# Kernel tuning notes

Hardware: AMD Instinct MI355X
Metric: run time of the kernel (lower is better)

The kernel has to match this reference:

```python
import jax, jax.numpy as jnp
import numpy as np

B, N, D, K = 32, 196, 1024, 512  # batch, tokens (14x14), feature dim, prototypes
EPS = 1e-8  # torch F.cosine_similarity default eps


def setup_inputs() -> dict:
    key = jax.random.key(0)
    ks = jax.random.split(key, 8)
    z = jax.random.normal(ks[0], (B, N, D), jnp.float32)
    prototypes = jax.random.normal(ks[1], (K, D), jnp.float32)  # nn.Parameter(randn)
    gate_w = jax.random.normal(ks[2], (2 * D, D), jnp.float32) * 0.02  # Linear(2D->D), stored [in,out]
    gate_b = jnp.zeros((D,), jnp.float32)
    dec_w = jax.random.normal(ks[3], (D, 7 * 7 * 512), jnp.float32) * 0.02
    dec_b = jnp.zeros((7 * 7 * 512,), jnp.float32)
    ct1_w = jax.random.normal(ks[4], (512, 256, 4, 4), jnp.float32) * 0.02  # torch [in,out,kh,kw]
    ct1_b = jnp.zeros((256,), jnp.float32)
    ct2_w = jax.random.normal(ks[5], (256, 3, 4, 4), jnp.float32) * 0.02
    ct2_b = jnp.zeros((3,), jnp.float32)
    return dict(z=z, prototypes=prototypes, gate_w=gate_w, gate_b=gate_b,
                dec_w=dec_w, dec_b=dec_b, ct1_w=ct1_w, ct1_b=ct1_b,
                ct2_w=ct2_w, ct2_b=ct2_b)


def _conv_transpose(x, w, b):
    # ConvTranspose2d(k=4, stride=2, pad=1) == conv with lhs_dilation=2,
    # padding k-1-pad=2, spatially-flipped kernel, torch weight layout [in,out,kh,kw] -> IOHW.
    wf = jnp.flip(w, (2, 3))
    y = jax.lax.conv_general_dilated(
        x, wf, window_strides=(1, 1), padding=((2, 2), (2, 2)),
        lhs_dilation=(2, 2), dimension_numbers=("NCHW", "IOHW", "NCHW"))
    return y + b[None, :, None, None]


def reference(z, prototypes, gate_w, gate_b, dec_w, dec_b, ct1_w, ct1_b, ct2_w, ct2_b):
    # MemoryBank: cosine similarity of every token against every prototype
    zn = jnp.linalg.norm(z, axis=-1, keepdims=True)            # [B,N,1]
    pn = jnp.linalg.norm(prototypes, axis=-1)                  # [K]
    dots = jnp.einsum('bnd,kd->bnk', z, prototypes)            # [B,N,K]
    sim = dots / jnp.maximum(zn * pn[None, None, :], EPS)
    attn = jax.nn.softmax(sim, axis=-1)                        # [B,N,K]
    z_hat = jnp.einsum('bnk,kd->bnd', attn, prototypes)        # [B,N,D]
    # GatedFusion: sigmoid gate over concat(z, z_hat)
    gate = jax.nn.sigmoid(jnp.concatenate([z, z_hat], axis=-1) @ gate_w + gate_b)
    z_fused = gate * z + (1.0 - gate) * z_hat                  # [B,N,D]
    # Decoder (original reshape is shape-inconsistent; pool tokens -> [B,D])
    pooled = z_fused.mean(axis=1)                              # [B,D]
    h = (pooled @ dec_w + dec_b).reshape(-1, 512, 7, 7)
    h = jax.nn.relu(_conv_transpose(h, ct1_w, ct1_b))          # [B,256,14,14]
    x_recon = _conv_transpose(h, ct2_w, ct2_b)                 # [B,3,28,28]
    return x_recon, attn
```

## Files before the change

kernel.cpp:

```cpp
#include <hip/hip_runtime.h>
#include <cstdint>
#include <cstddef>
#include <cmath>

#define EPS_COS 1e-8f

typedef unsigned short u16;
typedef __attribute__((ext_vector_type(8))) short short8v;
typedef __attribute__((ext_vector_type(4))) short short4v;
typedef __attribute__((ext_vector_type(4))) float f32x4;

__device__ __forceinline__ u16 f2bf(float x) {
    unsigned int u = __float_as_uint(x);
    return (u16)((u + 0x7FFFu + ((u >> 16) & 1u)) >> 16);
}
__device__ __forceinline__ float bf2f(u16 h) {
    return __uint_as_float(((unsigned int)h) << 16);
}

__global__ __launch_bounds__(256) void norm_cvt_kernel(const float* __restrict__ src,
                                                       u16* __restrict__ dst, int dstStride,
                                                       float* __restrict__ norms) {
    int r = blockIdx.x;
    int t = threadIdx.x;
    const float4 v = *reinterpret_cast<const float4*>(&src[(size_t)r * 1024 + t * 4]);
    short4v o;
    o[0] = f2bf(v.x); o[1] = f2bf(v.y); o[2] = f2bf(v.z); o[3] = f2bf(v.w);
    *reinterpret_cast<short4v*>(&dst[(size_t)r * dstStride + t * 4]) = o;
    float ss = v.x * v.x + v.y * v.y + v.z * v.z + v.w * v.w;
#pragma unroll
    for (int off = 32; off > 0; off >>= 1) ss += __shfl_down(ss, off);
    __shared__ float red[4];
    int wave = t >> 6, lane = t & 63;
    if (lane == 0) red[wave] = ss;
    __syncthreads();
    if (t == 0) norms[r] = sqrtf(red[0] + red[1] + red[2] + red[3]);
}

__global__ __launch_bounds__(256) void transpose_cvt_kernel(const float* __restrict__ src,
                                                            u16* __restrict__ dst,
                                                            int R, int C) {
    __shared__ float tile[64][65];
    int c0 = blockIdx.x * 64, r0 = blockIdx.y * 64;
    int t = threadIdx.x;
#pragma unroll
    for (int j = 0; j < 16; ++j) {
        int idx = j * 256 + t;
        int r = idx >> 6, c = idx & 63;
        tile[r][c] = src[(size_t)(r0 + r) * C + c0 + c];
    }
    __syncthreads();
#pragma unroll
    for (int j = 0; j < 16; ++j) {
        int idx = j * 256 + t;
        int c = idx >> 6, r = idx & 63;
        dst[(size_t)(c0 + c) * R + r0 + r] = f2bf(tile[r][c]);
    }
}

__global__ __launch_bounds__(256) void prep_kernel(u16* __restrict__ hp,
                                                   const float* __restrict__ ct1w,
                                                   u16* __restrict__ wt,
                                                   const float* __restrict__ ct2w,
                                                   u16* __restrict__ wpad,
                                                   float* __restrict__ pooled) {
    int idx = blockIdx.x * 256 + threadIdx.x;
    if (idx < 165888) {
        short8v zv = {0, 0, 0, 0, 0, 0, 0, 0};
        *reinterpret_cast<short8v*>(hp + (size_t)idx * 8) = zv;
    } else if (idx < 165888 + 131072) {
        int i = idx - 165888;
        int oc = i & 255, ic = i >> 8;
        float v[16];
#pragma unroll
        for (int j = 0; j < 16; ++j) v[j] = ct1w[(size_t)i * 16 + j];
#pragma unroll
        for (int pp = 0; pp < 4; ++pp) {
            int py = pp >> 1, px = pp & 1;
#pragma unroll
            for (int tap = 0; tap < 4; ++tap) {
                int ty = tap >> 1, tx = tap & 1;
                int ky = (1 - py) + 2 * ty;
                int kx = (1 - px) + 2 * tx;
                wt[((size_t)(pp * 256 + oc)) * 2048 + ic * 4 + tap] = f2bf(v[ky * 4 + kx]);
            }
        }
    } else if (idx < 165888 + 131072 + 16384) {
        int i = idx - 165888 - 131072;
        int ic = i & 255;
        int col = i >> 8;
        float v = 0.0f;
        if (col < 48) {
            int kx = col & 3, ky = (col >> 2) & 3, oc = col >> 4;
            v = ct2w[((size_t)ic * 3 + oc) * 16 + ky * 4 + kx];
        }
        wpad[i] = f2bf(v);
    } else {
        int i = idx - 165888 - 131072 - 16384;
        *reinterpret_cast<f32x4*>(pooled + (size_t)i * 4) = (f32x4){0.f, 0.f, 0.f, 0.f};
    }
}

template <int FM, int FN, int EPI, bool SWZ>
__global__ __launch_bounds__(256) void mfma_gemm_kernel(
    const u16* __restrict__ A, int sA, size_t zsA,
    const u16* __restrict__ B, int sB, size_t zsB,
    int M, int N, int K,
    float* __restrict__ Cf,
    u16* __restrict__ Cb, int sCb,
    const float* __restrict__ bias,
    const u16* __restrict__ zbf,
    const u16* __restrict__ zhbf, int szh,
    float* __restrict__ outf) {
    constexpr int BM = FM * 32, BN = FN * 32;
    constexpr int NA = BM / 32;
    constexpr int NB = BN / 32;
    __shared__ __align__(16) u16 As[BM * 64];
    __shared__ __align__(16) u16 Bs[BN * 64];
    int bx = blockIdx.x, by = blockIdx.y;
    if (SWZ) {
        int gx = gridDim.x;
        int nwg = gx * gridDim.y;
        int lb = by * gx + bx;
        int flat = (lb & 7) * (nwg >> 3) + (lb >> 3);
        bx = flat % gx;
        by = flat / gx;
    }
    A += (size_t)blockIdx.z * zsA;
    B += (size_t)blockIdx.z * zsB;
    const int t = threadIdx.x;
    const int lane = t & 63;
    const int wid = t >> 6;
    const int wm = wid >> 1, wn = wid & 1;
    const int m0 = bx * BM, n0 = by * BN;
    const int g = lane >> 4, lr = lane & 15;

    f32x4 acc[FM][FN];
#pragma unroll
    for (int i = 0; i < FM; ++i)
#pragma unroll
        for (int j = 0; j < FN; ++j) acc[i][j] = (f32x4){0.f, 0.f, 0.f, 0.f};

    short8v ra[NA], rb[NB];
#pragma unroll
    for (int j = 0; j < NA; ++j) {
        int c = j * 256 + t, row = c >> 3, ck = c & 7;
        ra[j] = *reinterpret_cast<const short8v*>(A + (size_t)(m0 + row) * sA + ck * 8);
    }
#pragma unroll
    for (int j = 0; j < NB; ++j) {
        int c = j * 256 + t, row = c >> 3, ck = c & 7;
        rb[j] = *reinterpret_cast<const short8v*>(B + (size_t)(n0 + row) * sB + ck * 8);
    }

    for (int k0 = 0; k0 < K; k0 += 64) {
        __syncthreads();
#pragma unroll
        for (int j = 0; j < NA; ++j) {
            int c = j * 256 + t, row = c >> 3, ck = c & 7;
            *reinterpret_cast<short8v*>(As + row * 64 + ((ck ^ (row & 7)) << 3)) = ra[j];
        }
#pragma unroll
        for (int j = 0; j < NB; ++j) {
            int c = j * 256 + t, row = c >> 3, ck = c & 7;
            *reinterpret_cast<short8v*>(Bs + row * 64 + ((ck ^ (row & 7)) << 3)) = rb[j];
        }
        __syncthreads();
        if (k0 + 64 < K) {
#pragma unroll
            for (int j = 0; j < NA; ++j) {
                int c = j * 256 + t, row = c >> 3, ck = c & 7;
                ra[j] = *reinterpret_cast<const short8v*>(A + (size_t)(m0 + row) * sA + k0 + 64 + ck * 8);
            }
#pragma unroll
            for (int j = 0; j < NB; ++j) {
                int c = j * 256 + t, row = c >> 3, ck = c & 7;
                rb[j] = *reinterpret_cast<const short8v*>(B + (size_t)(n0 + row) * sB + k0 + 64 + ck * 8);
            }
        }
#pragma unroll
        for (int kk = 0; kk < 2; ++kk) {
            short8v af[FM], bfr[FN];
#pragma unroll
            for (int fm = 0; fm < FM; ++fm) {
                int row = wm * (FM * 16) + fm * 16 + lr;
                int rc = (kk * 4 + g) ^ (row & 7);
                af[fm] = *reinterpret_cast<const short8v*>(As + row * 64 + rc * 8);
            }
#pragma unroll
            for (int fn = 0; fn < FN; ++fn) {
                int col = wn * (FN * 16) + fn * 16 + lr;
                int rc = (kk * 4 + g) ^ (col & 7);
                bfr[fn] = *reinterpret_cast<const short8v*>(Bs + col * 64 + rc * 8);
            }
#pragma unroll
            for (int fm = 0; fm < FM; ++fm)
#pragma unroll
                for (int fn = 0; fn < FN; ++fn)
                    acc[fm][fn] = __builtin_amdgcn_mfma_f32_16x16x32_bf16(
                        af[fm], bfr[fn], acc[fm][fn], 0, 0, 0);
        }
    }

    if (EPI == 2) {
#pragma unroll
        for (int fn = 0; fn < FN; ++fn) {
            int col = n0 + wn * (FN * 16) + fn * 16 + lr;
            int base = m0 + wm * (FM * 16) + g * 4;
            int b0 = base / 196;
            float p0 = 0.f, p1 = 0.f;
#pragma unroll
            for (int fm = 0; fm < FM; ++fm) {
#pragma unroll
                for (int r = 0; r < 4; ++r) {
                    int row = base + fm * 16 + r;
                    float v = acc[fm][fn][r];
                    float gs = 1.0f / (1.0f + __expf(-(v + bias[col])));
                    float zv = bf2f(zbf[(size_t)row * szh + col]);
                    float zh = bf2f(zhbf[(size_t)row * szh + col]);
                    float fused = gs * zv + (1.0f - gs) * zh;
                    bool same = (row / 196) == b0;
                    p0 += same ? fused : 0.f;
                    p1 += same ? 0.f : fused;
                }
            }
            atomicAdd(&outf[(size_t)b0 * 1024 + col], p0);
            if (p1 != 0.f) atomicAdd(&outf[(size_t)(b0 + 1) * 1024 + col], p1);
        }
    } else {
#pragma unroll
        for (int fm = 0; fm < FM; ++fm) {
#pragma unroll
            for (int fn = 0; fn < FN; ++fn) {
#pragma unroll
                for (int r = 0; r < 4; ++r) {
                    int row = m0 + wm * (FM * 16) + fm * 16 + g * 4 + r;
                    int col = n0 + wn * (FN * 16) + fn * 16 + lr;
                    float v = acc[fm][fn][r];
                    if (EPI == 0) {
                        Cf[(size_t)row * N + col] = v;
                    } else if (EPI == 1) {
                        Cb[(size_t)row * sCb + col] = f2bf(v);
                    } else {
                        if (row < 1568) {
                            float vv = fmaxf(v + bias[col], 0.0f);
                            int bb = row / 49, ss = row - bb * 49;
                            Cb[(((size_t)bb * 4 + blockIdx.z) * 49 + ss) * 256 + col] = f2bf(vv);
                        }
                    }
                }
            }
        }
    }
}

__global__ __launch_bounds__(256) void softmax_kernel(const float* __restrict__ dots,
                                                      const float* __restrict__ zn,
                                                      const float* __restrict__ pn,
                                                      float* __restrict__ attn,
                                                      u16* __restrict__ attn_bf) {
    int m = blockIdx.x;
    int t = threadIdx.x;
    float zm = zn[m];
    float d0 = dots[(size_t)m * 512 + t];
    float d1 = dots[(size_t)m * 512 + t + 256];
    float v0 = d0 / fmaxf(zm * pn[t], EPS_COS);
    float v1 = d1 / fmaxf(zm * pn[t + 256], EPS_COS);
    float mx = fmaxf(v0, v1);
#pragma unroll
    for (int off = 32; off > 0; off >>= 1) mx = fmaxf(mx, __shfl_down(mx, off));
    __shared__ float red[8];
    int wave = t >> 6, lane = t & 63;
    if (lane == 0) red[wave] = mx;
    __syncthreads();
    if (t == 0) red[4] = fmaxf(fmaxf(red[0], red[1]), fmaxf(red[2], red[3]));
    __syncthreads();
    mx = red[4];
    float e0 = expf(v0 - mx), e1 = expf(v1 - mx);
    float s = e0 + e1;
#pragma unroll
    for (int off = 32; off > 0; off >>= 1) s += __shfl_down(s, off);
    if (lane == 0) red[wave] = s;
    __syncthreads();
    if (t == 0) red[5] = 1.0f / (red[0] + red[1] + red[2] + red[3]);
    __syncthreads();
    float r = red[5];
    float a0 = e0 * r, a1 = e1 * r;
    attn[(size_t)m * 512 + t] = a0;
    attn[(size_t)m * 512 + t + 256] = a1;
    attn_bf[(size_t)m * 512 + t] = f2bf(a0);
    attn_bf[(size_t)m * 512 + t + 256] = f2bf(a1);
}

#define DEC_KC 64
__global__ __launch_bounds__(256) void dec_split_kernel(const float* __restrict__ pooled,
                                                        const float* __restrict__ dec_w,
                                                        float* __restrict__ partial) {
    const int t = threadIdx.x;
    const int lane = t & 63;
    const int wv = t >> 6;
    const int c = blockIdx.x * 256 + lane * 4;
    const int kc = blockIdx.y;
    __shared__ float pl[32][DEC_KC];
    for (int i = t; i < 32 * DEC_KC; i += 256) {
        int b = i >> 6, kk = i & (DEC_KC - 1);
        pl[b][kk] = pooled[(size_t)b * 1024 + kc * DEC_KC + kk] * (1.0f / 196.0f);
    }
    __syncthreads();
    f32x4 acc[8];
#pragma unroll
    for (int j = 0; j < 8; ++j) acc[j] = (f32x4){0.f, 0.f, 0.f, 0.f};
    const float* wp = dec_w + (size_t)(kc * DEC_KC) * 25088 + c;
#pragma unroll 8
    for (int k = 0; k < DEC_KC; ++k) {
        f32x4 w4 = *reinterpret_cast<const f32x4*>(wp + (size_t)k * 25088);
#pragma unroll
        for (int j = 0; j < 8; ++j) {
            float pv = pl[wv * 8 + j][k];
            acc[j].x = fmaf(pv, w4.x, acc[j].x);
            acc[j].y = fmaf(pv, w4.y, acc[j].y);
            acc[j].z = fmaf(pv, w4.z, acc[j].z);
            acc[j].w = fmaf(pv, w4.w, acc[j].w);
        }
    }
#pragma unroll
    for (int j = 0; j < 8; ++j) {
        int b = wv * 8 + j;
        *reinterpret_cast<f32x4*>(partial + ((size_t)kc * 32 + b) * 25088 + c) = acc[j];
    }
}

__global__ __launch_bounds__(256) void dec_reduce_kernel(const float* __restrict__ partial,
                                                         const float* __restrict__ dec_b,
                                                         u16* __restrict__ hp) {
    int c = blockIdx.x * 256 + threadIdx.x;
    int b = blockIdx.y;
    float s = dec_b[c];
#pragma unroll
    for (int kc = 0; kc < 16; ++kc)
        s += partial[((size_t)kc * 32 + b) * 25088 + c];
    int ic = c / 49, sp = c - ic * 49;
    int sy = sp / 7, sx = sp - sy * 7;
    hp[((size_t)b * 512 + ic) * 81 + (sy + 1) * 9 + sx + 1] = f2bf(s);
}

__global__ __launch_bounds__(256) void im2col_kernel(const u16* __restrict__ hp,
                                                     u16* __restrict__ A) {
    int idx = blockIdx.x * 256 + threadIdx.x;
    int k8 = idx & 255;
    int pr = idx >> 8;
    int p = pr / 1600;
    int row = pr - p * 1600;
    short8v o = {0, 0, 0, 0, 0, 0, 0, 0};
    if (row < 1568) {
        int b = row / 49, s = row - b * 49;
        int sy = s / 7, sx = s - sy * 7;
        int r0 = sy + (p >> 1) + 1;
        int c0 = sx + (p & 1) + 1;
        int ic0 = k8 * 2;
        const u16* hb = hp + ((size_t)b * 512 + ic0) * 81;
#pragma unroll
        for (int j = 0; j < 2; ++j) {
            o[j * 4 + 0] = hb[r0 * 9 + c0];
            o[j * 4 + 1] = hb[r0 * 9 + c0 - 1];
            o[j * 4 + 2] = hb[(r0 - 1) * 9 + c0];
            o[j * 4 + 3] = hb[(r0 - 1) * 9 + c0 - 1];
            hb += 81;
        }
    }
    *reinterpret_cast<short8v*>(A + (size_t)idx * 8) = o;
}

__global__ __launch_bounds__(256) void convt2_gather_kernel(const float* __restrict__ G,
                                                            const float* __restrict__ bias,
                                                            float* __restrict__ out) {
    int o = blockIdx.x * 256 + threadIdx.x;
    int ox = o % 28;
    int oy = (o / 28) % 28;
    int oc = (o / 784) % 3;
    int b = o / 2352;
    int by = (oy + 1) >> 1, bx = (ox + 1) >> 1;
    float acc = bias[oc];
#pragma unroll
    for (int ty = 0; ty < 2; ++ty) {
        int iy = by - ty;
        if ((unsigned)iy >= 14u) continue;
#pragma unroll
        for (int tx = 0; tx < 2; ++tx) {
            int ix = bx - tx;
            if ((unsigned)ix >= 14u) continue;
            int p = (iy & 1) * 2 + (ix & 1);
            int row = ((b * 4 + p) * 49) + (iy >> 1) * 7 + (ix >> 1);
            int ky = oy + 1 - 2 * iy, kx = ox + 1 - 2 * ix;
            acc += G[(size_t)row * 64 + oc * 16 + ky * 4 + kx];
        }
    }
    out[o] = acc;
}

extern "C" void kernel_launch(void* const* d_in, const int* in_sizes, int n_in,
                              void* d_out, int out_size, void* d_ws, size_t ws_size,
                              hipStream_t stream) {
    const float* z      = (const float*)d_in[0];
    const float* protos = (const float*)d_in[1];
    const float* gate_w = (const float*)d_in[2];
    const float* gate_b = (const float*)d_in[3];
    const float* dec_w  = (const float*)d_in[4];
    const float* dec_b  = (const float*)d_in[5];
    const float* ct1_w  = (const float*)d_in[6];
    const float* ct1_b  = (const float*)d_in[7];
    const float* ct2_w  = (const float*)d_in[8];
    const float* ct2_b  = (const float*)d_in[9];

    float* xout = (float*)d_out;
    float* attn = xout + 75264;

    float* w = (float*)d_ws;
    float* pn        = w;
    float* zn        = w + 512;
    float* pooled    = w + 6784;
    u16*   wt1bf     = (u16*)(w + 51840);
    u16*   protos_bf = (u16*)(w + 1100416);
    u16*   protosT   = (u16*)(w + 1362560);
    u16*   gwT       = (u16*)(w + 1624704);
    u16*   attn_bf   = (u16*)(w + 2673280);
    u16*   Abig      = (u16*)(w + 4278912);
    u16*   A_cls     = (u16*)(w + 2673280);
    float* dots      = w + 10701440;
    float* partial   = w + 4278912;
    u16*   h2cb      = (u16*)(w + 11364992);
    u16*   hp        = (u16*)(w + 17123968);
    float* G         = w + 17787520;
    u16*   wpad      = (u16*)(w + 18188928);

    prep_kernel<<<1256, 256, 0, stream>>>(hp, ct1_w, wt1bf, ct2_w, wpad, pooled);
    norm_cvt_kernel<<<6272, 256, 0, stream>>>(z, Abig, 2048, zn);
    norm_cvt_kernel<<<512, 256, 0, stream>>>(protos, protos_bf, 1024, pn);
    transpose_cvt_kernel<<<dim3(16, 8), 256, 0, stream>>>(protos, protosT, 512, 1024);
    transpose_cvt_kernel<<<dim3(16, 32), 256, 0, stream>>>(gate_w, gwT, 2048, 1024);
    mfma_gemm_kernel<2, 4, 0, true><<<dim3(98, 4), 256, 0, stream>>>(
        Abig, 2048, 0, protos_bf, 1024, 0, 6272, 512, 1024,
        dots, nullptr, 0, nullptr, nullptr, nullptr, 0, nullptr);
    softmax_kernel<<<6272, 256, 0, stream>>>(dots, zn, pn, attn, attn_bf);
    mfma_gemm_kernel<4, 4, 1, true><<<dim3(49, 8), 256, 0, stream>>>(
        attn_bf, 512, 0, protosT, 512, 0, 6272, 1024, 512,
        nullptr, Abig + 1024, 2048, nullptr, nullptr, nullptr, 0, nullptr);
    mfma_gemm_kernel<4, 4, 2, true><<<dim3(49, 8), 256, 0, stream>>>(
        Abig, 2048, 0, gwT, 2048, 0, 6272, 1024, 2048,
        nullptr, nullptr, 0, gate_b, Abig, Abig + 1024, 2048, pooled);
    dec_split_kernel<<<dim3(98, 16), 256, 0, stream>>>(pooled, dec_w, partial);
    dec_reduce_kernel<<<dim3(98, 32), 256, 0, stream>>>(partial, dec_b, hp);
    im2col_kernel<<<6400, 256, 0, stream>>>(hp, A_cls);
    mfma_gemm_kernel<2, 2, 3, false><<<dim3(25, 4, 4), 256, 0, stream>>>(
        A_cls, 2048, (size_t)1600 * 2048, wt1bf, 2048, (size_t)256 * 2048,
        1600, 256, 2048, nullptr, h2cb, 0, ct1_b, nullptr, nullptr, 0, nullptr);
    mfma_gemm_kernel<2, 2, 0, false><<<dim3(98, 1), 256, 0, stream>>>(
        h2cb, 256, 0, wpad, 256, 0, 6272, 64, 256,
        G, nullptr, 0, nullptr, nullptr, nullptr, 0, nullptr);
    convt2_gather_kernel<<<294, 256, 0, stream>>>(G, ct2_b, xout);
}
```

Baseline: 207.8 us.

## Replace split-K decoder linear with single MFMA bf16 GEMM kernel

Replaces the fp32 split-K decoder projection and its separate reduction kernel with one kernel. That kernel converts pooled features and dec_w to bf16 in shared memory, runs MFMA 16x16x32, and writes biased outputs straight into the padded hp buffer. This drops the partial-sum round trip through global memory and one launch, while still streaming the 100MB dec_w once. It also shrinks the M tile of the two conv-transpose GEMMs to launch more blocks. Rounding dec_w and pooled to bf16 adds precision loss.

```diff
diff --git a/kernel.cpp b/kernel.cpp
--- a/kernel.cpp
+++ b/kernel.cpp
@@ -254,6 +254,107 @@
     }
 }
 
+__global__ __launch_bounds__(256) void dec_gemm_kernel(const float* __restrict__ pooled,
+                                                       const float* __restrict__ dec_w,
+                                                       const float* __restrict__ dec_b,
+                                                       u16* __restrict__ hp) {
+    __shared__ __align__(16) u16 As[32 * 72];
+    __shared__ __align__(16) u16 Bs[128 * 72];
+    const int t = threadIdx.x;
+    const int lane = t & 63;
+    const int wid = t >> 6;
+    const int wm = wid >> 1, wn = wid & 1;
+    const int n0 = blockIdx.x * 128;
+    const int g = lane >> 4, lr = lane & 15;
+
+    const int ar = t >> 3;
+    const int ak = (t & 7) * 8;
+    const int bn4 = (t & 31) * 4;
+    const int bk4 = (t >> 5) * 4;
+    const int bswz = ((bn4 >> 2) & 3) << 3;
+    const int bkp = (bk4 ^ bswz);
+
+    f32x4 acc[4];
+#pragma unroll
+    for (int j = 0; j < 4; ++j) acc[j] = (f32x4){0.f, 0.f, 0.f, 0.f};
+
+    f32x4 ra[2];
+    f32x4 rb[2][4];
+#pragma unroll
+    for (int h = 0; h < 2; ++h)
+        ra[h] = *reinterpret_cast<const f32x4*>(pooled + ar * 1024 + ak + h * 4);
+#pragma unroll
+    for (int q = 0; q < 2; ++q)
+#pragma unroll
+        for (int i = 0; i < 4; ++i)
+            rb[q][i] = *reinterpret_cast<const f32x4*>(
+                dec_w + (size_t)(bk4 + q * 32 + i) * 25088 + n0 + bn4);
+
+    for (int k0 = 0; k0 < 1024; k0 += 64) {
+        __syncthreads();
+        {
+            short8v o;
+#pragma unroll
+            for (int h = 0; h < 2; ++h) {
+                o[h * 4 + 0] = f2bf(ra[h].x * (1.0f / 196.0f));
+                o[h * 4 + 1] = f2bf(ra[h].y * (1.0f / 196.0f));
+                o[h * 4 + 2] = f2bf(ra[h].z * (1.0f / 196.0f));
+                o[h * 4 + 3] = f2bf(ra[h].w * (1.0f / 196.0f));
+            }
+            *reinterpret_cast<short8v*>(As + ar * 72 + ak) = o;
+        }
+#pragma unroll
+        for (int q = 0; q < 2; ++q) {
+#pragma unroll
+            for (int j = 0; j < 4; ++j) {
+                short4v o4;
+                o4[0] = f2bf(rb[q][0][j]);
+                o4[1] = f2bf(rb[q][1][j]);
+                o4[2] = f2bf(rb[q][2][j]);
+                o4[3] = f2bf(rb[q][3][j]);
+                *reinterpret_cast<short4v*>(Bs + (bn4 + j) * 72 + bkp + q * 32) = o4;
+            }
+        }
+        __syncthreads();
+        if (k0 + 64 < 1024) {
+#pragma unroll
+            for (int h = 0; h < 2; ++h)
+                ra[h] = *reinterpret_cast<const f32x4*>(
+                    pooled + ar * 1024 + k0 + 64 + ak + h * 4);
+#pragma unroll
+            for (int q = 0; q < 2; ++q)
+#pragma unroll
+                for (int i = 0; i < 4; ++i)
+                    rb[q][i] = *reinterpret_cast<const f32x4*>(
+                        dec_w + (size_t)(k0 + 64 + bk4 + q * 32 + i) * 25088 + n0 + bn4);
+        }
+#pragma unroll
+        for (int kk = 0; kk < 2; ++kk) {
+            int row = wm * 16 + lr;
+            short8v af = *reinterpret_cast<const short8v*>(As + row * 72 + kk * 32 + g * 8);
+#pragma unroll
+            for (int fn = 0; fn < 4; ++fn) {
+                int col = wn * 64 + fn * 16 + lr;
+                int ch = (kk * 32 + g * 8) ^ (((col >> 2) & 3) << 3);
+                short8v bf8 = *reinterpret_cast<const short8v*>(Bs + col * 72 + ch);
+                acc[fn] = __builtin_amdgcn_mfma_f32_16x16x32_bf16(af, bf8, acc[fn], 0, 0, 0);
+            }
+        }
+    }
+#pragma unroll
+    for (int fn = 0; fn < 4; ++fn) {
+#pragma unroll
+        for (int r = 0; r < 4; ++r) {
+            int row = wm * 16 + g * 4 + r;
+            int col = n0 + wn * 64 + fn * 16 + lr;
+            float v = acc[fn][r] + dec_b[col];
+            int ic = col / 49, sp = col - ic * 49;
+            int sy = sp / 7, sx = sp - sy * 7;
+            hp[((size_t)row * 512 + ic) * 81 + (sy + 1) * 9 + sx + 1] = f2bf(v);
+        }
+    }
+}
+
 __global__ __launch_bounds__(256) void softmax_kernel(const float* __restrict__ dots,
                                                       const float* __restrict__ zn,
                                                       const float* __restrict__ pn,
@@ -290,58 +391,6 @@
     attn[(size_t)m * 512 + t + 256] = a1;
     attn_bf[(size_t)m * 512 + t] = f2bf(a0);
     attn_bf[(size_t)m * 512 + t + 256] = f2bf(a1);
-}
-
-#define DEC_KC 64
-__global__ __launch_bounds__(256) void dec_split_kernel(const float* __restrict__ pooled,
-                                                        const float* __restrict__ dec_w,
-                                                        float* __restrict__ partial) {
-    const int t = threadIdx.x;
-    const int lane = t & 63;
-    const int wv = t >> 6;
-    const int c = blockIdx.x * 256 + lane * 4;
-    const int kc = blockIdx.y;
-    __shared__ float pl[32][DEC_KC];
-    for (int i = t; i < 32 * DEC_KC; i += 256) {
-        int b = i >> 6, kk = i & (DEC_KC - 1);
-        pl[b][kk] = pooled[(size_t)b * 1024 + kc * DEC_KC + kk] * (1.0f / 196.0f);
-    }
-    __syncthreads();
-    f32x4 acc[8];
-#pragma unroll
-    for (int j = 0; j < 8; ++j) acc[j] = (f32x4){0.f, 0.f, 0.f, 0.f};
-    const float* wp = dec_w + (size_t)(kc * DEC_KC) * 25088 + c;
-#pragma unroll 8
-    for (int k = 0; k < DEC_KC; ++k) {
-        f32x4 w4 = *reinterpret_cast<const f32x4*>(wp + (size_t)k * 25088);
-#pragma unroll
-        for (int j = 0; j < 8; ++j) {
-            float pv = pl[wv * 8 + j][k];
-            acc[j].x = fmaf(pv, w4.x, acc[j].x);
-            acc[j].y = fmaf(pv, w4.y, acc[j].y);
-            acc[j].z = fmaf(pv, w4.z, acc[j].z);
-            acc[j].w = fmaf(pv, w4.w, acc[j].w);
-        }
-    }
-#pragma unroll
-    for (int j = 0; j < 8; ++j) {
-        int b = wv * 8 + j;
-        *reinterpret_cast<f32x4*>(partial + ((size_t)kc * 32 + b) * 25088 + c) = acc[j];
-    }
-}
-
-__global__ __launch_bounds__(256) void dec_reduce_kernel(const float* __restrict__ partial,
-                                                         const float* __restrict__ dec_b,
-                                                         u16* __restrict__ hp) {
-    int c = blockIdx.x * 256 + threadIdx.x;
-    int b = blockIdx.y;
-    float s = dec_b[c];
-#pragma unroll
-    for (int kc = 0; kc < 16; ++kc)
-        s += partial[((size_t)kc * 32 + b) * 25088 + c];
-    int ic = c / 49, sp = c - ic * 49;
-    int sy = sp / 7, sx = sp - sy * 7;
-    hp[((size_t)b * 512 + ic) * 81 + (sy + 1) * 9 + sx + 1] = f2bf(s);
 }
 
 __global__ __launch_bounds__(256) void im2col_kernel(const u16* __restrict__ hp,
@@ -427,7 +476,6 @@
     u16*   Abig      = (u16*)(w + 4278912);
     u16*   A_cls     = (u16*)(w + 2673280);
     float* dots      = w + 10701440;
-    float* partial   = w + 4278912;
     u16*   h2cb      = (u16*)(w + 11364992);
     u16*   hp        = (u16*)(w + 17123968);
     float* G         = w + 17787520;
@@ -448,13 +496,12 @@
     mfma_gemm_kernel<4, 4, 2, true><<<dim3(49, 8), 256, 0, stream>>>(
         Abig, 2048, 0, gwT, 2048, 0, 6272, 1024, 2048,
         nullptr, nullptr, 0, gate_b, Abig, Abig + 1024, 2048, pooled);
-    dec_split_kernel<<<dim3(98, 16), 256, 0, stream>>>(pooled, dec_w, partial);
-    dec_reduce_kernel<<<dim3(98, 32), 256, 0, stream>>>(partial, dec_b, hp);
+    dec_gemm_kernel<<<196, 256, 0, stream>>>(pooled, dec_w, dec_b, hp);
     im2col_kernel<<<6400, 256, 0, stream>>>(hp, A_cls);
-    mfma_gemm_kernel<2, 2, 3, false><<<dim3(25, 4, 4), 256, 0, stream>>>(
+    mfma_gemm_kernel<1, 2, 3, false><<<dim3(50, 4, 4), 256, 0, stream>>>(
         A_cls, 2048, (size_t)1600 * 2048, wt1bf, 2048, (size_t)256 * 2048,
         1600, 256, 2048, nullptr, h2cb, 0, ct1_b, nullptr, nullptr, 0, nullptr);
-    mfma_gemm_kernel<2, 2, 0, false><<<dim3(98, 1), 256, 0, stream>>>(
+    mfma_gemm_kernel<1, 2, 0, false><<<dim3(196, 1), 256, 0, stream>>>(
         h2cb, 256, 0, wpad, 256, 0, 6272, 64, 256,
         G, nullptr, 0, nullptr, nullptr, nullptr, 0, nullptr);
     convt2_gather_kernel<<<294, 256, 0, stream>>>(G, ct2_b, xout);
```

Measured after the change: 189.6 us. 8.8% less time.
